# Performance work log

Hardware: AMD Instinct MI355X
Metric: run time of the kernel (lower is better)

Reference implementation:

```python
import jax, jax.numpy as jnp
import numpy as np

B, S, E, H = 8, 1024, 1024, 16  # batch, seq, embed, heads; head_dim = E//H = 64

def setup_inputs() -> dict:
    key = jax.random.key(0)
    k1, k2, k3 = jax.random.split(key, 3)
    x = jax.random.normal(k1, (B, S, E), dtype=jnp.float32)
    W_attn = jax.random.normal(k2, (E, 3 * E), dtype=jnp.float32) * (1.0 / np.sqrt(E))
    W_proj = jax.random.normal(k3, (E, E), dtype=jnp.float32) * (1.0 / np.sqrt(E))
    return {"x": x, "W_attn": W_attn, "W_proj": W_proj}

def reference(x, W_attn, W_proj):
    b, s, e = x.shape
    d = e // H
    qkv = x @ W_attn                      # [b, s, 3e]
    q, k, v = jnp.split(qkv, 3, axis=-1)
    q = q.reshape(b, s, H, d)
    k = k.reshape(b, s, H, d)
    v = v.reshape(b, s, H, d)
    scale = 1.0 / np.sqrt(d).astype(np.float32)
    scores = jnp.einsum('bqhd,bkhd->bhqk', q, k) * scale  # [b, H, s, s]
    causal = jnp.tril(jnp.ones((s, s), dtype=bool))
    scores = jnp.where(causal[None, None, :, :], scores, -jnp.inf)
    attn = jax.nn.softmax(scores, axis=-1)
    y = jnp.einsum('bhqk,bkhd->bqhd', attn, v).reshape(b, s, e)
    return y @ W_proj
```

## Files before the change

kernel.cpp:

```cpp
#include <hip/hip_runtime.h>
#include <hip/hip_bf16.h>

typedef unsigned short u16;
typedef __attribute__((ext_vector_type(8))) short short8;
typedef __attribute__((ext_vector_type(4))) float f32x4;
typedef __attribute__((ext_vector_type(16))) float f32x16;
typedef __attribute__((ext_vector_type(4))) unsigned short u16x4;

#define DEVINL __device__ __forceinline__

DEVINL u16 f2bf(float f) {
    union { float f; unsigned u; } x; x.f = f;
    unsigned u = x.u;
    u += 0x7fffu + ((u >> 16) & 1u);
    return (u16)(u >> 16);
}

DEVINL void gload_lds16(const void* g, void* l) {
    __builtin_amdgcn_global_load_lds(
        (const __attribute__((address_space(1))) unsigned*)g,
        (__attribute__((address_space(3))) unsigned*)l, 16, 0, 0);
}

DEVINL int swz(int row) { return (((row & 7) ^ ((row >> 3) & 7)) << 4); }

DEVINL void swap32(unsigned& a, unsigned& b) {
#if __has_builtin(__builtin_amdgcn_permlane32_swap)
    typedef __attribute__((ext_vector_type(2))) unsigned uv2;
    uv2 r = __builtin_amdgcn_permlane32_swap(a, b, false, false);
    a = r.x; b = r.y;
#else
    int h = ((int)(threadIdx.x & 63)) >> 5;
    unsigned pa = (unsigned)__shfl_xor((int)a, 32);
    unsigned pb = (unsigned)__shfl_xor((int)b, 32);
    unsigned na = h ? pb : a;
    unsigned nb = h ? b : pa;
    a = na; b = nb;
#endif
}

__global__ void k_conv_x(const float* __restrict__ in, u16* __restrict__ out, int n4) {
    int i = blockIdx.x * blockDim.x + threadIdx.x;
    int stride = gridDim.x * blockDim.x;
    for (; i < n4; i += stride) {
        float4 v = ((const float4*)in)[i];
        u16x4 o;
        o.x = f2bf(v.x); o.y = f2bf(v.y); o.z = f2bf(v.z); o.w = f2bf(v.w);
        ((u16x4*)out)[i] = o;
    }
}

__global__ void k_transpose_bf(const float* __restrict__ in, u16* __restrict__ out, int R, int C) {
    __shared__ float t[32][33];
    int c0 = blockIdx.x * 32, r0 = blockIdx.y * 32;
    int tx = threadIdx.x, ty = threadIdx.y;
    #pragma unroll
    for (int j = 0; j < 32; j += 8)
        t[ty + j][tx] = in[(size_t)(r0 + ty + j) * C + c0 + tx];
    __syncthreads();
    #pragma unroll
    for (int j = 0; j < 32; j += 8)
        out[(size_t)(c0 + ty + j) * R + r0 + tx] = f2bf(t[tx][ty + j]);
}

template<bool OUT_BF16>
__global__ __launch_bounds__(256, 2)
void k_gemm2(const u16* __restrict__ A, const u16* __restrict__ BT,
             void* __restrict__ C, int N, int K) {
    __shared__ char lds[2 * 32768];

    const int tid  = threadIdx.x;
    const int lane = tid & 63;
    const int lo   = lane & 15;
    const int hi   = lane >> 4;
    const int wave = tid >> 6;
    const int wm   = wave >> 1;
    const int wn   = wave & 1;

    const int gx   = gridDim.x;
    const int nwg  = gx * gridDim.y;
    const int orig = blockIdx.y * gx + blockIdx.x;
    const int wg   = (orig & 7) * (nwg >> 3) + (orig >> 3);
    const long row0 = (long)(wg / gx) * 128;
    const long col0 = (long)(wg % gx) * 128;

    const int NT = K >> 6;

    const int srow = tid >> 3;
    const int gsb  = ((tid & 7) ^ (srow & 7)) << 4;

    auto stage = [&](int t) {
        char* base = lds + (t & 1) * 32768;
        #pragma unroll
        for (int c = 0; c < 4; c++)
            gload_lds16((const char*)(A + (row0 + c * 32 + srow) * (size_t)K + t * 64) + gsb,
                        base + c * 4096 + tid * 16);
        #pragma unroll
        for (int c = 0; c < 4; c++)
            gload_lds16((const char*)(BT + (col0 + c * 32 + srow) * (size_t)K + t * 64) + gsb,
                        base + 16384 + c * 4096 + tid * 16);
    };

    f32x4 acc[4][4] = {};

    stage(0);
    asm volatile("s_waitcnt vmcnt(0)" ::: "memory");
    __builtin_amdgcn_s_barrier();

    for (int t = 0; t < NT; t++) {
        if (t + 1 < NT) stage(t + 1);
        const char* ab = lds + (t & 1) * 32768;
        const char* bb = ab + 16384;
        #pragma unroll
        for (int kk = 0; kk < 2; kk++) {
            short8 af[4], bf[4];
            #pragma unroll
            for (int m = 0; m < 4; m++) {
                int r = wm * 64 + m * 16 + lo;
                af[m] = *(const short8*)(ab + r * 128 + ((kk * 64 + hi * 16) ^ ((r & 7) << 4)));
            }
            #pragma unroll
            for (int n = 0; n < 4; n++) {
                int r = wn * 64 + n * 16 + lo;
                bf[n] = *(const short8*)(bb + r * 128 + ((kk * 64 + hi * 16) ^ ((r & 7) << 4)));
            }
            #pragma unroll
            for (int m = 0; m < 4; m++)
                #pragma unroll
                for (int n = 0; n < 4; n++)
                    acc[m][n] = __builtin_amdgcn_mfma_f32_16x16x32_bf16(af[m], bf[n], acc[m][n], 0, 0, 0);
        }
        if (t + 1 < NT) {
            asm volatile("s_waitcnt vmcnt(0)" ::: "memory");
            __builtin_amdgcn_s_barrier();
        }
    }

    #pragma unroll
    for (int m = 0; m < 4; m++)
        #pragma unroll
        for (int n = 0; n < 4; n++)
            #pragma unroll
            for (int r = 0; r < 4; r++) {
                long row = row0 + wm * 64 + m * 16 + hi * 4 + r;
                long col = col0 + wn * 64 + n * 16 + lo;
                if constexpr (OUT_BF16)
                    ((u16*)C)[row * (size_t)N + col] = f2bf(acc[m][n][r]);
                else
                    ((float*)C)[row * (size_t)N + col] = acc[m][n][r];
            }
}

#define SCALE_L2E 0.18033688011112042f

__global__ __launch_bounds__(256, 2)
void k_attn(const u16* __restrict__ qkv, u16* __restrict__ y) {
    constexpr int S = 1024, E = 1024, TE = 3072;
    __shared__ u16 Kt[64 * 64];
    __shared__ u16 Vt[64 * 64];

    const int tid  = threadIdx.x;
    const int lane = tid & 63;
    const int l31  = lane & 31;
    const int hA   = lane >> 5;
    const int wave = tid >> 6;

    const int qi = 7 - (int)(blockIdx.x >> 7);
    const int bh = blockIdx.x & 127;
    const int b  = bh >> 4;
    const int h  = bh & 15;
    const int q0 = qi * 128;
    const size_t rowbase = (size_t)b * S;
    const int qg = q0 + wave * 32 + l31;

    short8 qf[4];
    {
        const u16* qp = qkv + (rowbase + qg) * TE + h * 64 + hA * 8;
        #pragma unroll
        for (int kd = 0; kd < 4; kd++) qf[kd] = *(const short8*)(qp + kd * 16);
    }

    f32x16 o0 = {}, o1 = {};
    float ms = -1e30f, lsum = 0.f;

    const int kr0 = (wave << 3) + (lane >> 3);
    const int kcb = (lane & 7) * 16;
    const int vkv = (tid >> 3) * 2;
    const int vdc = (tid & 7) * 8;

    const int ntiles = 2 * qi + 2;
    for (int t = 0; t < ntiles; ++t) {
        const int kv0 = t * 64;
        __syncthreads();
        #pragma unroll
        for (int it = 0; it < 2; it++) {
            int r = kr0 + it * 32;
            const char* src = (const char*)qkv
                + (((rowbase + kv0 + r) * TE + E + h * 64) << 1) + (kcb ^ swz(r));
            gload_lds16(src, (char*)Kt + wave * 1024 + it * 4096);
        }
        {
            const u16* vsrc = qkv + (rowbase + kv0 + vkv) * TE + 2 * E + h * 64 + vdc;
            short8 v0 = *(const short8*)vsrc;
            short8 v1 = *(const short8*)(vsrc + TE);
            #pragma unroll
            for (int j = 0; j < 8; j++) {
                int d = vdc + j;
                unsigned val = (unsigned)(u16)v0[j] | ((unsigned)(u16)v1[j] << 16);
                *(unsigned*)((char*)Vt + d * 128 + ((vkv * 2) ^ swz(d))) = val;
            }
        }
        __syncthreads();

        const bool active = (kv0 <= q0 + wave * 32 + 31);
        if (!active) continue;

        f32x16 s0 = {}, s1 = {};
        #pragma unroll
        for (int kd = 0; kd < 4; kd++) {
            int r0 = l31, r1 = 32 + l31;
            short8 ka0 = *(const short8*)((const char*)Kt + r0 * 128 + ((kd * 32 + hA * 16) ^ swz(r0)));
            short8 ka1 = *(const short8*)((const char*)Kt + r1 * 128 + ((kd * 32 + hA * 16) ^ swz(r1)));
            s0 = __builtin_amdgcn_mfma_f32_32x32x16_bf16(ka0, qf[kd], s0, 0, 0, 0);
            s1 = __builtin_amdgcn_mfma_f32_32x32x16_bf16(ka1, qf[kd], s1, 0, 0, 0);
        }

        if (kv0 + 63 > q0 + wave * 32) {
            #pragma unroll
            for (int r = 0; r < 16; r++) {
                int kvr = kv0 + ((r & 3) + 8 * (r >> 2) + 4 * hA);
                if (kvr > qg)      s0[r] = -1e30f;
                if (kvr + 32 > qg) s1[r] = -1e30f;
            }
        }

        float pm = s0[0];
        #pragma unroll
        for (int r = 1; r < 16; r++) pm = fmaxf(pm, s0[r]);
        #pragma unroll
        for (int r = 0; r < 16; r++) pm = fmaxf(pm, s1[r]);
        pm = fmaxf(pm, __shfl_xor(pm, 32));
        float pms = pm * SCALE_L2E;
        if (__any(pms - ms > 8.0f)) {
            float msn = fmaxf(ms, pms);
            float alpha = exp2f(ms - msn);
            ms = msn;
            lsum *= alpha;
            #pragma unroll
            for (int r = 0; r < 16; r++) { o0[r] *= alpha; o1[r] *= alpha; }
        }

        float part = 0.f;
        #pragma unroll
        for (int r = 0; r < 16; r++) {
            float p0 = exp2f(s0[r] * SCALE_L2E - ms);
            float p1 = exp2f(s1[r] * SCALE_L2E - ms);
            s0[r] = p0; s1[r] = p1;
            part += p0 + p1;
        }
        lsum += part + __shfl_xor(part, 32);

        unsigned w0[8], w1[8];
        #pragma unroll
        for (int j = 0; j < 8; j++) {
            asm("v_cvt_pk_bf16_f32 %0, %1, %2" : "=v"(w0[j]) : "v"(s0[2 * j]), "v"(s0[2 * j + 1]));
            asm("v_cvt_pk_bf16_f32 %0, %1, %2" : "=v"(w1[j]) : "v"(s1[2 * j]), "v"(s1[2 * j + 1]));
        }

        #define PV_TILE(W, ST)                                                              \
        {                                                                                   \
            _Pragma("unroll")                                                               \
            for (int kkl = 0; kkl < 2; kkl++) {                                             \
                unsigned a  = W[4 * kkl],     bsw = W[4 * kkl + 2];                         \
                unsigned a2 = W[4 * kkl + 1], b2  = W[4 * kkl + 3];                         \
                swap32(a, bsw); swap32(a2, b2);                                             \
                union { int4 i; short8 s; } u;                                              \
                u.i = make_int4((int)a, (int)a2, (int)bsw, (int)b2);                        \
                {                                                                           \
                    int row = l31;                                                          \
                    short8 va = *(const short8*)((const char*)Vt + row * 128                \
                                  + (((ST) * 64 + kkl * 32 + hA * 16) ^ swz(row)));         \
                    o0 = __builtin_amdgcn_mfma_f32_32x32x16_bf16(va, u.s, o0, 0, 0, 0);     \
                }                                                                           \
                {                                                                           \
                    int row = 32 + l31;                                                     \
                    short8 va = *(const short8*)((const char*)Vt + row * 128                \
                                  + (((ST) * 64 + kkl * 32 + hA * 16) ^ swz(row)));         \
                    o1 = __builtin_amdgcn_mfma_f32_32x32x16_bf16(va, u.s, o1, 0, 0, 0);     \
                }                                                                           \
            }                                                                               \
        }
        PV_TILE(w0, 0)
        PV_TILE(w1, 1)
        #undef PV_TILE
    }

    __syncthreads();
    float rinv = 1.0f / lsum;
    u16* Ot = (wave < 2 ? Kt : Vt) + (wave & 1) * 2048;
    const int X = (l31 & 7) << 4;
    #pragma unroll
    for (int rq = 0; rq < 4; rq++) {
        u16x4 pk0, pk1;
        #pragma unroll
        for (int j = 0; j < 4; j++) {
            pk0[j] = f2bf(o0[4 * rq + j] * rinv);
            pk1[j] = f2bf(o1[4 * rq + j] * rinv);
        }
        *(u16x4*)((char*)Ot + l31 * 128 + ((16 * rq + 8 * hA) ^ X))      = pk0;
        *(u16x4*)((char*)Ot + l31 * 128 + ((64 + 16 * rq + 8 * hA) ^ X)) = pk1;
    }
    __syncthreads();
    #pragma unroll
    for (int p = 0; p < 4; p++) {
        int row = p * 8 + (lane >> 3);
        int cc  = lane & 7;
        short8 vv = *(const short8*)((const char*)Ot + row * 128
                      + ((cc * 16) ^ ((row & 7) << 4)));
        *(short8*)(y + (rowbase + q0 + wave * 32 + row) * E + h * 64 + cc * 8) = vv;
    }
}

extern "C" void kernel_launch(void* const* d_in, const int* in_sizes, int n_in,
                              void* d_out, int out_size, void* d_ws, size_t ws_size,
                              hipStream_t stream) {
    const float* x     = (const float*)d_in[0];
    const float* Wattn = (const float*)d_in[1];
    const float* Wproj = (const float*)d_in[2];
    float* out = (float*)d_out;

    char* ws = (char*)d_ws;
    u16* buf0 = (u16*)ws;
    u16* wT   = (u16*)(ws + 16777216);
    u16* qkv  = (u16*)(ws + 16777216 + 6291456);

    k_conv_x<<<2048, 256, 0, stream>>>(x, buf0, 8388608 / 4);
    k_transpose_bf<<<dim3(3072 / 32, 1024 / 32), dim3(32, 8), 0, stream>>>(Wattn, wT, 1024, 3072);
    k_gemm2<true><<<dim3(3072 / 128, 8192 / 128), 256, 0, stream>>>(buf0, wT, qkv, 3072, 1024);
    k_transpose_bf<<<dim3(1024 / 32, 1024 / 32), dim3(32, 8), 0, stream>>>(Wproj, wT, 1024, 1024);
    k_attn<<<dim3(1024), 256, 0, stream>>>(qkv, buf0);
    k_gemm2<false><<<dim3(1024 / 128, 8192 / 128), 256, 0, stream>>>(buf0, wT, out, 1024, 1024);
}
```

Baseline: 133.7 us.

## Triple-buffer GEMM LDS pipeline with K-tile 32 and partial vmcnt waits

The bf16 GEMM moves from a double-buffered K=64 tile to a triple-buffered K=32 tile, with a new swizzle for 64-byte rows. Loads are issued two stages ahead, and each iteration waits only for the older stage (vmcnt(4)) before its barrier. This lets global-to-LDS copies overlap compute more deeply. LDS per block drops to 48KB and launch bounds rise to 3 blocks per CU for higher occupancy, at the cost of twice as many barriers and fewer MFMAs per barrier.

Result: slower. 146.9 us (+9.9%).

```diff
diff --git a/kernel.cpp b/kernel.cpp
--- a/kernel.cpp
+++ b/kernel.cpp
@@ -64,10 +64,10 @@
 }
 
 template<bool OUT_BF16>
-__global__ __launch_bounds__(256, 2)
-void k_gemm2(const u16* __restrict__ A, const u16* __restrict__ BT,
+__global__ __launch_bounds__(256, 3)
+void k_gemm3(const u16* __restrict__ A, const u16* __restrict__ BT,
              void* __restrict__ C, int N, int K) {
-    __shared__ char lds[2 * 32768];
+    __shared__ char lds[3 * 16384];
 
     const int tid  = threadIdx.x;
     const int lane = tid & 63;
@@ -84,56 +84,60 @@
     const long row0 = (long)(wg / gx) * 128;
     const long col0 = (long)(wg % gx) * 128;
 
-    const int NT = K >> 6;
-
-    const int srow = tid >> 3;
-    const int gsb  = ((tid & 7) ^ (srow & 7)) << 4;
+    const int NT = K >> 5;
+
+    const int sr = tid >> 2;
+    const int sb = (tid & 3) * 16;
 
     auto stage = [&](int t) {
-        char* base = lds + (t & 1) * 32768;
-        #pragma unroll
-        for (int c = 0; c < 4; c++)
-            gload_lds16((const char*)(A + (row0 + c * 32 + srow) * (size_t)K + t * 64) + gsb,
+        char* base = lds + (t % 3) * 16384;
+        #pragma unroll
+        for (int c = 0; c < 2; c++) {
+            int r   = c * 64 + sr;
+            int src = sb ^ ((r & 3) << 4);
+            gload_lds16((const char*)(A + (row0 + r) * (size_t)K + t * 32) + src,
                         base + c * 4096 + tid * 16);
-        #pragma unroll
-        for (int c = 0; c < 4; c++)
-            gload_lds16((const char*)(BT + (col0 + c * 32 + srow) * (size_t)K + t * 64) + gsb,
-                        base + 16384 + c * 4096 + tid * 16);
+        }
+        #pragma unroll
+        for (int c = 0; c < 2; c++) {
+            int r   = c * 64 + sr;
+            int src = sb ^ ((r & 3) << 4);
+            gload_lds16((const char*)(BT + (col0 + r) * (size_t)K + t * 32) + src,
+                        base + 8192 + c * 4096 + tid * 16);
+        }
     };
 
     f32x4 acc[4][4] = {};
 
     stage(0);
-    asm volatile("s_waitcnt vmcnt(0)" ::: "memory");
-    __builtin_amdgcn_s_barrier();
+    stage(1);
+
+    const int xs = (lo & 3) << 4;
 
     for (int t = 0; t < NT; t++) {
-        if (t + 1 < NT) stage(t + 1);
-        const char* ab = lds + (t & 1) * 32768;
-        const char* bb = ab + 16384;
-        #pragma unroll
-        for (int kk = 0; kk < 2; kk++) {
-            short8 af[4], bf[4];
-            #pragma unroll
-            for (int m = 0; m < 4; m++) {
-                int r = wm * 64 + m * 16 + lo;
-                af[m] = *(const short8*)(ab + r * 128 + ((kk * 64 + hi * 16) ^ ((r & 7) << 4)));
-            }
-            #pragma unroll
-            for (int n = 0; n < 4; n++) {
-                int r = wn * 64 + n * 16 + lo;
-                bf[n] = *(const short8*)(bb + r * 128 + ((kk * 64 + hi * 16) ^ ((r & 7) << 4)));
-            }
-            #pragma unroll
-            for (int m = 0; m < 4; m++)
-                #pragma unroll
-                for (int n = 0; n < 4; n++)
-                    acc[m][n] = __builtin_amdgcn_mfma_f32_16x16x32_bf16(af[m], bf[n], acc[m][n], 0, 0, 0);
-        }
-        if (t + 1 < NT) {
-            asm volatile("s_waitcnt vmcnt(0)" ::: "memory");
-            __builtin_amdgcn_s_barrier();
-        }
+        if (t + 1 < NT) asm volatile("s_waitcnt vmcnt(4)" ::: "memory");
+        else            asm volatile("s_waitcnt vmcnt(0)" ::: "memory");
+        __builtin_amdgcn_s_barrier();
+        if (t + 2 < NT) stage(t + 2);
+
+        const char* ab = lds + (t % 3) * 16384;
+        const char* bb = ab + 8192;
+        short8 af[4], bf[4];
+        #pragma unroll
+        for (int m = 0; m < 4; m++) {
+            int r = wm * 64 + m * 16 + lo;
+            af[m] = *(const short8*)(ab + r * 64 + ((hi * 16) ^ xs));
+        }
+        #pragma unroll
+        for (int n = 0; n < 4; n++) {
+            int r = wn * 64 + n * 16 + lo;
+            bf[n] = *(const short8*)(bb + r * 64 + ((hi * 16) ^ xs));
+        }
+        #pragma unroll
+        for (int m = 0; m < 4; m++)
+            #pragma unroll
+            for (int n = 0; n < 4; n++)
+                acc[m][n] = __builtin_amdgcn_mfma_f32_16x16x32_bf16(af[m], bf[n], acc[m][n], 0, 0, 0);
     }
 
     #pragma unroll
@@ -336,8 +340,8 @@
 
     k_conv_x<<<2048, 256, 0, stream>>>(x, buf0, 8388608 / 4);
     k_transpose_bf<<<dim3(3072 / 32, 1024 / 32), dim3(32, 8), 0, stream>>>(Wattn, wT, 1024, 3072);
-    k_gemm2<true><<<dim3(3072 / 128, 8192 / 128), 256, 0, stream>>>(buf0, wT, qkv, 3072, 1024);
+    k_gemm3<true><<<dim3(3072 / 128, 8192 / 128), 256, 0, stream>>>(buf0, wT, qkv, 3072, 1024);
     k_transpose_bf<<<dim3(1024 / 32, 1024 / 32), dim3(32, 8), 0, stream>>>(Wproj, wT, 1024, 1024);
     k_attn<<<dim3(1024), 256, 0, stream>>>(qkv, buf0);
-    k_gemm2<false><<<dim3(1024 / 128, 8192 / 128), 256, 0, stream>>>(buf0, wT, out, 1024, 1024);
-}
+    k_gemm3<false><<<dim3(1024 / 128, 8192 / 128), 256, 0, stream>>>(buf0, wT, out, 1024, 1024);
+}
```

## Double-buffer K/V tiles in attention kernel to overlap loads with compute

Applied to the files above, without the earlier changes.

Splits shared memory into two K/V buffers and prefetches tile t+1 while tile t is computed. This drops one barrier per iteration and aims to hide global-load latency behind the MFMA work. The V prefetch still goes through registers, so its global load may stall before the LDS writes and limit how much overlap is gained. LDS use per block doubles to 32KB.

After: 134.7 us. About the same (+0.8%).

```diff
diff --git a/kernel.cpp b/kernel.cpp
--- a/kernel.cpp
+++ b/kernel.cpp
@@ -156,8 +156,7 @@
 __global__ __launch_bounds__(256, 2)
 void k_attn(const u16* __restrict__ qkv, u16* __restrict__ y) {
     constexpr int S = 1024, E = 1024, TE = 3072;
-    __shared__ u16 Kt[64 * 64];
-    __shared__ u16 Vt[64 * 64];
+    __shared__ char alds[2 * 16384];
 
     const int tid  = threadIdx.x;
     const int lane = tid & 63;
@@ -188,29 +187,36 @@
     const int vkv = (tid >> 3) * 2;
     const int vdc = (tid & 7) * 8;
 
-    const int ntiles = 2 * qi + 2;
-    for (int t = 0; t < ntiles; ++t) {
+    auto stage = [&](int t) {
+        char* base = alds + (t & 1) * 16384;
         const int kv0 = t * 64;
-        __syncthreads();
         #pragma unroll
         for (int it = 0; it < 2; it++) {
             int r = kr0 + it * 32;
             const char* src = (const char*)qkv
                 + (((rowbase + kv0 + r) * TE + E + h * 64) << 1) + (kcb ^ swz(r));
-            gload_lds16(src, (char*)Kt + wave * 1024 + it * 4096);
-        }
-        {
-            const u16* vsrc = qkv + (rowbase + kv0 + vkv) * TE + 2 * E + h * 64 + vdc;
-            short8 v0 = *(const short8*)vsrc;
-            short8 v1 = *(const short8*)(vsrc + TE);
-            #pragma unroll
-            for (int j = 0; j < 8; j++) {
-                int d = vdc + j;
-                unsigned val = (unsigned)(u16)v0[j] | ((unsigned)(u16)v1[j] << 16);
-                *(unsigned*)((char*)Vt + d * 128 + ((vkv * 2) ^ swz(d))) = val;
-            }
-        }
+            gload_lds16(src, base + wave * 1024 + it * 4096);
+        }
+        const u16* vsrc = qkv + (rowbase + kv0 + vkv) * TE + 2 * E + h * 64 + vdc;
+        short8 v0 = *(const short8*)vsrc;
+        short8 v1 = *(const short8*)(vsrc + TE);
+        #pragma unroll
+        for (int j = 0; j < 8; j++) {
+            int d = vdc + j;
+            unsigned val = (unsigned)(u16)v0[j] | ((unsigned)(u16)v1[j] << 16);
+            *(unsigned*)(base + 8192 + d * 128 + ((vkv * 2) ^ swz(d))) = val;
+        }
+    };
+
+    const int ntiles = 2 * qi + 2;
+    stage(0);
+    for (int t = 0; t < ntiles; ++t) {
         __syncthreads();
+        if (t + 1 < ntiles) stage(t + 1);
+
+        const char* Kt = alds + (t & 1) * 16384;
+        const char* Vt = Kt + 8192;
+        const int kv0 = t * 64;
 
         const bool active = (kv0 <= q0 + wave * 32 + 31);
         if (!active) continue;
@@ -219,8 +225,8 @@
         #pragma unroll
         for (int kd = 0; kd < 4; kd++) {
             int r0 = l31, r1 = 32 + l31;
-            short8 ka0 = *(const short8*)((const char*)Kt + r0 * 128 + ((kd * 32 + hA * 16) ^ swz(r0)));
-            short8 ka1 = *(const short8*)((const char*)Kt + r1 * 128 + ((kd * 32 + hA * 16) ^ swz(r1)));
+            short8 ka0 = *(const short8*)(Kt + r0 * 128 + ((kd * 32 + hA * 16) ^ swz(r0)));
+            short8 ka1 = *(const short8*)(Kt + r1 * 128 + ((kd * 32 + hA * 16) ^ swz(r1)));
             s0 = __builtin_amdgcn_mfma_f32_32x32x16_bf16(ka0, qf[kd], s0, 0, 0, 0);
             s1 = __builtin_amdgcn_mfma_f32_32x32x16_bf16(ka1, qf[kd], s1, 0, 0, 0);
         }
@@ -278,13 +284,13 @@
                 u.i = make_int4((int)a, (int)a2, (int)bsw, (int)b2);                        \
                 {                                                                           \
                     int row = l31;                                                          \
-                    short8 va = *(const short8*)((const char*)Vt + row * 128                \
+                    short8 va = *(const short8*)(Vt + row * 128                             \
                                   + (((ST) * 64 + kkl * 32 + hA * 16) ^ swz(row)));         \
                     o0 = __builtin_amdgcn_mfma_f32_32x32x16_bf16(va, u.s, o0, 0, 0, 0);     \
                 }                                                                           \
                 {                                                                           \
                     int row = 32 + l31;                                                     \
-                    short8 va = *(const short8*)((const char*)Vt + row * 128                \
+                    short8 va = *(const short8*)(Vt + row * 128                             \
                                   + (((ST) * 64 + kkl * 32 + hA * 16) ^ swz(row)));         \
                     o1 = __builtin_amdgcn_mfma_f32_32x32x16_bf16(va, u.s, o1, 0, 0, 0);     \
                 }                                                                           \
@@ -297,7 +303,7 @@
 
     __syncthreads();
     float rinv = 1.0f / lsum;
-    u16* Ot = (wave < 2 ? Kt : Vt) + (wave & 1) * 2048;
+    char* Ot = alds + wave * 4096;
     const int X = (l31 & 7) << 4;
     #pragma unroll
     for (int rq = 0; rq < 4; rq++) {
@@ -307,16 +313,15 @@
             pk0[j] = f2bf(o0[4 * rq + j] * rinv);
             pk1[j] = f2bf(o1[4 * rq + j] * rinv);
         }
-        *(u16x4*)((char*)Ot + l31 * 128 + ((16 * rq + 8 * hA) ^ X))      = pk0;
-        *(u16x4*)((char*)Ot + l31 * 128 + ((64 + 16 * rq + 8 * hA) ^ X)) = pk1;
+        *(u16x4*)(Ot + l31 * 128 + ((16 * rq + 8 * hA) ^ X))      = pk0;
+        *(u16x4*)(Ot + l31 * 128 + ((64 + 16 * rq + 8 * hA) ^ X)) = pk1;
     }
     __syncthreads();
     #pragma unroll
     for (int p = 0; p < 4; p++) {
         int row = p * 8 + (lane >> 3);
         int cc  = lane & 7;
-        short8 vv = *(const short8*)((const char*)Ot + row * 128
-                      + ((cc * 16) ^ ((row & 7) << 4)));
+        short8 vv = *(const short8*)(Ot + row * 128 + ((cc * 16) ^ ((row & 7) << 4)));
         *(short8*)(y + (rowbase + q0 + wave * 32 + row) * E + h * 64 + cc * 8) = vv;
     }
 }
```
